# Optimization experiments

Hardware: AMD Instinct MI355X
Metric: run time of the kernel (lower is better)

The kernel has to match this reference:

```python
import jax, jax.numpy as jnp
import numpy as np

NUM_NODES = 20000
NUM_EDGES = 1_000_000
NUM_REL = 12        # internal num_relation (init arg 24 // 2)
NUM_STEP = 6
HID = 128
B_SET = 64          # number of unique (h, r) queries
BS, NEG = 64, 32    # scoring batch
EPS = 1e-10


def setup_inputs() -> dict:
    key = jax.random.key(0)
    ks = jax.random.split(key, 16)
    s = 0.1
    inp = {
        "query_emb": jax.random.normal(ks[0], (2 * NUM_REL + 1, HID), jnp.float32) * s,
        "w_ih": jax.random.normal(ks[1], (4 * HID, HID), jnp.float32) * s,
        "w_hh": jax.random.normal(ks[2], (4 * HID, HID), jnp.float32) * s,
        "b_ih": jax.random.normal(ks[3], (4 * HID,), jnp.float32) * s,
        "b_hh": jax.random.normal(ks[4], (4 * HID,), jnp.float32) * s,
        "wl_w": jax.random.normal(ks[5], (2 * NUM_REL, HID), jnp.float32) * s,
        "wl_b": jax.random.normal(ks[6], (2 * NUM_REL,), jnp.float32) * s,
        "lin_w": jax.random.normal(ks[7], (1, 1), jnp.float32),
        "lin_b": jax.random.normal(ks[8], (1,), jnp.float32),
        "edge_index": jax.random.randint(ks[9], (2, NUM_EDGES), 0, NUM_NODES, jnp.int64),
        "edge_type": jax.random.randint(ks[10], (NUM_EDGES,), 0, 2 * NUM_REL, jnp.int64),
        "h_set": jax.random.randint(ks[11], (B_SET,), 0, NUM_NODES, jnp.int64),
        "r_set": jax.random.randint(ks[12], (B_SET,), 0, NUM_REL, jnp.int64),
        "t_index": jax.random.randint(ks[13], (BS, NEG), 0, NUM_NODES, jnp.int64),
        "hr_inverse": jax.random.randint(ks[14], (BS, NEG), 0, B_SET, jnp.int64),
    }
    return inp


def _lstm(query, w_ih, w_hh, b_ih, b_hh):
    # query: [T, B, D]; single-layer PyTorch LSTM (gate order i, f, g, o)
    B, D = query.shape[1], w_hh.shape[1]
    h0 = jnp.zeros((B, D), query.dtype)

    def step(carry, x):
        h, c = carry
        gates = x @ w_ih.T + b_ih + h @ w_hh.T + b_hh
        i, f, g, o = jnp.split(gates, 4, axis=-1)
        c = jax.nn.sigmoid(f) * c + jax.nn.sigmoid(i) * jnp.tanh(g)
        h = jax.nn.sigmoid(o) * jnp.tanh(c)
        return (h, c), h

    _, hidden = jax.lax.scan(step, (h0, h0), query)
    return hidden  # [T, B, D]


def reference(query_emb, w_ih, w_hh, b_ih, b_hh, wl_w, wl_b, lin_w, lin_b,
              edge_index, edge_type, h_set, r_set, t_index, hr_inverse):
    N1 = NUM_NODES + 1
    B = h_set.shape[0]
    # query sequence: relation repeated (T-1) times, then END token (= NUM_REL)
    q_index = jnp.concatenate(
        [jnp.tile(r_set[None, :], (NUM_STEP - 1, 1)),
         jnp.full((1, B), NUM_REL, dtype=r_set.dtype)], axis=0)  # [T, B]
    query = query_emb[q_index]                                   # [T, B, D]
    hidden = _lstm(query, w_ih, w_hh, b_ih, b_hh)                # [T, B, D]

    memory = jax.nn.one_hot(h_set, N1, dtype=query_emb.dtype)[None]  # [1, B, N1]
    node_in, node_out = edge_index[0], edge_index[1]

    output = None
    for i in range(NUM_STEP):
        k = hidden[i]                 # [B, D]
        v = hidden[: i + 1]           # [i+1, B, D]
        attn = jax.nn.softmax(jnp.einsum('bd,tbd->bt', k, v), axis=-1)
        inp = jnp.einsum('bt,tbn->nb', attn, memory)             # [N1, B]
        weight = jax.nn.softmax(k @ wl_w.T + wl_b, axis=-1).T    # [2R, B]
        # gather -> weight -> scatter_add over edges (edge_weight == 1)
        message = inp[node_in] * weight[edge_type]               # [E, B]
        output = jax.ops.segment_sum(message, node_out, num_segments=N1)
        output = output / jnp.maximum(output.sum(0, keepdims=True), EPS)
        memory = jnp.concatenate([memory, output.T[None]], axis=0)

    score = output[t_index, hr_inverse]           # [BS, NEG]
    return score * lin_w[0, 0] + lin_b[0]
```

## Files before the change

kernel.cpp:

```cpp
#include <hip/hip_runtime.h>
#include <hip/hip_fp16.h>
#include <math.h>

namespace {

constexpr int kN1 = 20001;
constexpr int kNE = 1000000;
constexpr int kNStep = 6;
constexpr int kHid = 128;
constexpr int kB = 64;
constexpr int kNRel2 = 24;
constexpr float kEps = 1e-10f;
constexpr unsigned kSent = (unsigned)kN1;
constexpr int kPMax = kNE + 8 * kN1;
constexpr int kGatherBlocks = 2048;
constexpr int kNWaves = kGatherBlocks * 4;

__device__ __forceinline__ float sig(float x) { return 1.0f / (1.0f + expf(-x)); }

__device__ __forceinline__ float2 cvt2(unsigned u) {
  __half2 h = *reinterpret_cast<__half2*>(&u);
  return __half22float2(h);
}


__global__ __launch_bounds__(256) void lstm_kernel(
    const float* __restrict__ query_emb, const float* __restrict__ w_ih,
    const float* __restrict__ w_hh, const float* __restrict__ b_ih,
    const float* __restrict__ b_hh, const int* __restrict__ r_set,
    float* __restrict__ hidden ) {
  const int b = blockIdx.x;
  const int tid = threadIdx.x;
  __shared__ float xs[kHid], hs[kHid], cs[kHid], gates[4 * kHid];
  if (tid < kHid) { hs[tid] = 0.f; cs[tid] = 0.f; }
  __syncthreads();
  for (int s = 0; s < kNStep; ++s) {
    const int q = (s < kNStep - 1) ? r_set[b] : 12;
    if (tid < kHid) xs[tid] = query_emb[q * kHid + tid];
    __syncthreads();
    for (int j = tid; j < 4 * kHid; j += blockDim.x) {
      const float* wi = &w_ih[j * kHid];
      const float* wh = &w_hh[j * kHid];
      float a = b_ih[j] + b_hh[j];
#pragma unroll 4
      for (int k = 0; k < kHid; ++k) a += xs[k] * wi[k] + hs[k] * wh[k];
      gates[j] = a;
    }
    __syncthreads();
    if (tid < kHid) {
      const float ig = sig(gates[tid]);
      const float fg = sig(gates[kHid + tid]);
      const float gg = tanhf(gates[2 * kHid + tid]);
      const float og = sig(gates[3 * kHid + tid]);
      const float cn = fg * cs[tid] + ig * gg;
      const float hn = og * tanhf(cn);
      cs[tid] = cn;
      hs[tid] = hn;
      hidden[(s * kB + b) * kHid + tid] = hn;
    }
    __syncthreads();
  }
}

__global__ __launch_bounds__(128) void attn_weight_kernel(
    const float* __restrict__ hidden, const float* __restrict__ wl_w,
    const float* __restrict__ wl_b, float* __restrict__ attnAll ,
    float* __restrict__ weightAll ) {
  const int b = blockIdx.x;
  const int tid = threadIdx.x;
  __shared__ float hsm[kNStep][kHid];
  __shared__ float G[kNStep][kNStep];
  __shared__ float logits[kNStep][kNRel2];
  for (int s = 0; s < kNStep; ++s) hsm[s][tid] = hidden[(s * kB + b) * kHid + tid];
  __syncthreads();
  if (tid < 36) {
    const int i = tid / 6, t = tid % 6;
    if (t <= i) {
      float acc = 0.f;
      for (int k = 0; k < kHid; ++k) acc += hsm[i][k] * hsm[t][k];
      G[i][t] = acc;
    }
  }
  for (int p = tid; p < kNStep * kNRel2; p += 128) {
    const int i = p / kNRel2, r = p % kNRel2;
    float acc = wl_b[r];
    for (int k = 0; k < kHid; ++k) acc += hsm[i][k] * wl_w[r * kHid + k];
    logits[i][r] = acc;
  }
  __syncthreads();
  if (tid < kNStep) {
    const int i = tid;
    float m = G[i][0];
    for (int t = 1; t <= i; ++t) m = fmaxf(m, G[i][t]);
    float ssum = 0.f;
    float ev[kNStep];
    for (int t = 0; t <= i; ++t) { ev[t] = expf(G[i][t] - m); ssum += ev[t]; }
    for (int t = 0; t <= i; ++t) attnAll[(i * kNStep + t) * kB + b] = ev[t] / ssum;
    float mw = logits[i][0];
    for (int r = 1; r < kNRel2; ++r) mw = fmaxf(mw, logits[i][r]);
    float sw = 0.f;
    float ew[kNRel2];
    for (int r = 0; r < kNRel2; ++r) { ew[r] = expf(logits[i][r] - mw); sw += ew[r]; }
    for (int r = 0; r < kNRel2; ++r) weightAll[(i * kNRel2 + r) * kB + b] = ew[r] / sw;
  }
}


__global__ __launch_bounds__(256) void zero_kernel(int* __restrict__ counts,
                                                   float* __restrict__ colsumAll) {
  const int i = blockIdx.x * blockDim.x + threadIdx.x;
  if (i < kN1) counts[i] = 0;
  if (i < kNStep * kB) colsumAll[i] = 0.f;
}

__global__ __launch_bounds__(256) void hist_kernel(const int* __restrict__ nout,
                                                   int* __restrict__ counts) {
  for (int e = blockIdx.x * blockDim.x + threadIdx.x; e < kNE;
       e += gridDim.x * blockDim.x)
    atomicAdd(&counts[nout[e]], 1);
}

__global__ __launch_bounds__(1024) void scan_kernel(const int* __restrict__ counts,
                                                    int* __restrict__ poffsets,
                                                    int* __restrict__ cursor) {
  __shared__ int part[1024];
  const int tid = threadIdx.x;
  const int chunk = (kN1 + 1023) / 1024;
  const int beg = tid * chunk;
  const int end = min(beg + chunk, kN1);
  int s = 0;
  for (int i = beg; i < end; ++i) s += (counts[i] + 7) & ~7;
  part[tid] = s;
  __syncthreads();
  for (int off = 1; off < 1024; off <<= 1) {
    const int v = (tid >= off) ? part[tid - off] : 0;
    __syncthreads();
    part[tid] += v;
    __syncthreads();
  }
  int run = part[tid] - s;
  for (int i = beg; i < end; ++i) {
    poffsets[i] = run;
    cursor[i] = run;
    run += (counts[i] + 7) & ~7;
  }
  if (tid == 1023) poffsets[kN1] = part[1023];
}

__global__ __launch_bounds__(256) void fill_kernel(unsigned* __restrict__ packed) {
  for (int i = blockIdx.x * blockDim.x + threadIdx.x; i < kPMax;
       i += gridDim.x * blockDim.x)
    packed[i] = kSent;
}

__global__ __launch_bounds__(256) void permute_kernel(
    const int* __restrict__ nin, const int* __restrict__ nout,
    const int* __restrict__ etype, int* __restrict__ cursor,
    unsigned* __restrict__ packed) {
  for (int e = blockIdx.x * blockDim.x + threadIdx.x; e < kNE;
       e += gridDim.x * blockDim.x) {
    const int d = nout[e];
    const int pos = atomicAdd(&cursor[d], 1);
    packed[pos] = (unsigned)nin[e] | ((unsigned)etype[e] << 15);
  }
}


__global__ __launch_bounds__(256) void inp_kernel(
    const float* __restrict__ attnAll, const float* __restrict__ colsumAll,
    const int* __restrict__ h_set, const float* __restrict__ outs,
    __half* __restrict__ inp, int step) {
  __shared__ float coef[kNStep][kB];
  __shared__ int hsm[kB];
  const int tid = threadIdx.x;
  for (int j = tid; j < kNStep * kB; j += 256) {
    const int t = j >> 6, b = j & 63;
    float c = 0.f;
    if (t == 0)
      c = attnAll[(step * kNStep) * kB + b];
    else if (t <= step)
      c = attnAll[(step * kNStep + t) * kB + b] /
          fmaxf(colsumAll[(t - 1) * kB + b], kEps);
    coef[t][b] = c;
  }
  if (tid < kB) hsm[tid] = h_set[tid];
  __syncthreads();
  const int total = (kN1 + 1) * 16;
  for (int idx = blockIdx.x * blockDim.x + tid; idx < total;
       idx += gridDim.x * blockDim.x) {
    const int n = idx >> 4;
    const int cg = idx & 15;
    float ax = 0.f, ay = 0.f, az = 0.f, aw = 0.f;
    if (n < kN1) {
      for (int t = 1; t <= step; ++t) {
        const float4 ct = *reinterpret_cast<const float4*>(&coef[t][cg * 4]);
        const float4 o = *reinterpret_cast<const float4*>(
            &outs[((long long)(t - 1) * kN1 + n) * kB + cg * 4]);
        ax += ct.x * o.x; ay += ct.y * o.y; az += ct.z * o.z; aw += ct.w * o.w;
      }
      const int c0 = cg * 4;
      if (hsm[c0 + 0] == n) ax += coef[0][c0 + 0];
      if (hsm[c0 + 1] == n) ay += coef[0][c0 + 1];
      if (hsm[c0 + 2] == n) az += coef[0][c0 + 2];
      if (hsm[c0 + 3] == n) aw += coef[0][c0 + 3];
    }
    __half2 h0 = __floats2half2_rn(ax, ay);
    __half2 h1 = __floats2half2_rn(az, aw);
    uint2 u;
    u.x = *reinterpret_cast<unsigned*>(&h0);
    u.y = *reinterpret_cast<unsigned*>(&h1);
    *reinterpret_cast<uint2*>(inp + (long long)idx * 4) = u;
  }
}

__global__ __launch_bounds__(256) void gather_seg_kernel(
    const __half* __restrict__ inp ,
    const float* __restrict__ weight ,
    const unsigned* __restrict__ packed, const int* __restrict__ poffsets,
    float* __restrict__ out, float* __restrict__ colsum) {
  __shared__ __align__(16) __half wsm[kNRel2 * kB];
  __shared__ float red[4][kB];
  const int tid = threadIdx.x;
  const int lane = tid & 63;
  const int wid = tid >> 6;
  const int g = lane >> 3;
  const int cb = lane & 7;
  for (int j = tid; j < kNRel2 * kB; j += 256) wsm[j] = __float2half(weight[j]);
  __syncthreads();

  float csum[8] = {0.f, 0.f, 0.f, 0.f, 0.f, 0.f, 0.f, 0.f};
  const int wave = blockIdx.x * 4 + wid;
  const int P = poffsets[kN1];
  const int nG = P >> 3;
  const int chunkG = (nG + kNWaves - 1) / kNWaves;
  const int gbeg = wave * chunkG;
  if (gbeg < nG) {
    const int gend = min(gbeg + chunkG, nG);
    auto lb = [&](int x) {
      int lo = 0, hi = kN1;
      while (lo < hi) {
        const int mid = (lo + hi) >> 1;
        if (poffsets[mid] < x) lo = mid + 1; else hi = mid;
      }
      return lo;
    };
    const int nbeg = lb(gbeg * 8);
    const int nend = (gend >= nG) ? kN1 : lb(gend * 8);
    if (nbeg < nend) {
      float acc[8] = {0.f, 0.f, 0.f, 0.f, 0.f, 0.f, 0.f, 0.f};
      int n = nbeg;
      int nextB = poffsets[n + 1];
      const int ebeg = poffsets[nbeg];
      const int eend = poffsets[nend];
      for (int ebase = ebeg; ebase < eend; ebase += 8) {
        while (ebase >= nextB) {
#pragma unroll
          for (int j = 0; j < 8; ++j) {
            acc[j] += __shfl_xor(acc[j], 8);
            acc[j] += __shfl_xor(acc[j], 16);
            acc[j] += __shfl_xor(acc[j], 32);
          }
          if (g == 0) {
            *reinterpret_cast<float4*>(out + (long long)n * kB + cb * 8) =
                make_float4(acc[0], acc[1], acc[2], acc[3]);
            *reinterpret_cast<float4*>(out + (long long)n * kB + cb * 8 + 4) =
                make_float4(acc[4], acc[5], acc[6], acc[7]);
#pragma unroll
            for (int j = 0; j < 8; ++j) csum[j] += acc[j];
          }
#pragma unroll
          for (int j = 0; j < 8; ++j) acc[j] = 0.f;
          ++n;
          nextB = poffsets[n + 1];
        }
        const unsigned p = packed[ebase + g];
        const int src = (int)(p & 0x7fffu);
        const int et = (int)(p >> 15);
        const uint4 v4 =
            *reinterpret_cast<const uint4*>(inp + (long long)src * kB + cb * 8);
        const uint4 w4 = *reinterpret_cast<const uint4*>(wsm + et * kB + cb * 8);
        const float2 v0 = cvt2(v4.x), v1 = cvt2(v4.y), v2 = cvt2(v4.z), v3 = cvt2(v4.w);
        const float2 w0 = cvt2(w4.x), w1 = cvt2(w4.y), w2 = cvt2(w4.z), w3 = cvt2(w4.w);
        acc[0] += v0.x * w0.x; acc[1] += v0.y * w0.y;
        acc[2] += v1.x * w1.x; acc[3] += v1.y * w1.y;
        acc[4] += v2.x * w2.x; acc[5] += v2.y * w2.y;
        acc[6] += v3.x * w3.x; acc[7] += v3.y * w3.y;
      }
      while (n < nend) {
#pragma unroll
        for (int j = 0; j < 8; ++j) {
          acc[j] += __shfl_xor(acc[j], 8);
          acc[j] += __shfl_xor(acc[j], 16);
          acc[j] += __shfl_xor(acc[j], 32);
        }
        if (g == 0) {
          *reinterpret_cast<float4*>(out + (long long)n * kB + cb * 8) =
              make_float4(acc[0], acc[1], acc[2], acc[3]);
          *reinterpret_cast<float4*>(out + (long long)n * kB + cb * 8 + 4) =
              make_float4(acc[4], acc[5], acc[6], acc[7]);
#pragma unroll
          for (int j = 0; j < 8; ++j) csum[j] += acc[j];
        }
#pragma unroll
        for (int j = 0; j < 8; ++j) acc[j] = 0.f;
        ++n;
      }
    }
  }
  if (g == 0) {
#pragma unroll
    for (int j = 0; j < 8; ++j) red[wid][cb * 8 + j] = csum[j];
  }
  __syncthreads();
  if (wid == 0) {
    const float r = red[0][lane] + red[1][lane] + red[2][lane] + red[3][lane];
    unsafeAtomicAdd(&colsum[lane], r);
  }
}

__global__ __launch_bounds__(256) void score_kernel(
    const float* __restrict__ outLast, const float* __restrict__ colsumLast,
    const int* __restrict__ t_index, const int* __restrict__ hr_inverse,
    const float* __restrict__ lin_w, const float* __restrict__ lin_b,
    float* __restrict__ out, int n) {
  const int i = blockIdx.x * blockDim.x + threadIdx.x;
  if (i < n) {
    const int node = t_index[i];
    const int b = hr_inverse[i];
    const float v = outLast[(long long)node * kB + b] / fmaxf(colsumLast[b], kEps);
    out[i] = v * lin_w[0] + lin_b[0];
  }
}


__global__ __launch_bounds__(256) void inp_zero_kernel(
    const float* __restrict__ attnAll, const int* __restrict__ h_set,
    const float* __restrict__ outs, float* __restrict__ inp,
    float* __restrict__ out_next, float* __restrict__ colsum, int step) {
  const long long total = (long long)kN1 * kB;
  for (long long idx = (long long)blockIdx.x * blockDim.x + threadIdx.x; idx < total;
       idx += (long long)gridDim.x * blockDim.x) {
    const int b = (int)(idx & 63);
    const int n = (int)(idx >> 6);
    float acc = (h_set[b] == n) ? attnAll[(step * kNStep) * kB + b] : 0.f;
    for (int t = 1; t <= step; ++t)
      acc += attnAll[(step * kNStep + t) * kB + b] *
             outs[(long long)(t - 1) * kN1 * kB + idx];
    inp[idx] = acc;
    out_next[idx] = 0.f;
  }
  if (blockIdx.x == 0 && threadIdx.x < kB) colsum[threadIdx.x] = 0.f;
}

__global__ __launch_bounds__(256) void scatter_kernel(
    const float* __restrict__ inp, const float* __restrict__ weight,
    const int* __restrict__ nin, const int* __restrict__ nout,
    const int* __restrict__ etype, float* __restrict__ out,
    float* __restrict__ colsum) {
  const int lane = threadIdx.x & 63;
  const int wave = blockIdx.x * (blockDim.x >> 6) + (threadIdx.x >> 6);
  const int nwave = gridDim.x * (blockDim.x >> 6);
  __shared__ float wsm[kNRel2 * kB];
  for (int j = threadIdx.x; j < kNRel2 * kB; j += blockDim.x) wsm[j] = weight[j];
  __syncthreads();
  float csum = 0.f;
  for (int e = wave; e < kNE; e += nwave) {
    const float v = inp[(long long)nin[e] * kB + lane] * wsm[etype[e] * kB + lane];
    unsafeAtomicAdd(&out[(long long)nout[e] * kB + lane], v);
    csum += v;
  }
  unsafeAtomicAdd(&colsum[lane], csum);
}

__global__ __launch_bounds__(256) void normalize_kernel(
    float* __restrict__ out, const float* __restrict__ colsum) {
  const long long total = (long long)kN1 * kB;
  for (long long idx = (long long)blockIdx.x * blockDim.x + threadIdx.x; idx < total;
       idx += (long long)gridDim.x * blockDim.x)
    out[idx] /= fmaxf(colsum[idx & 63], kEps);
}

__global__ __launch_bounds__(256) void score_kernel_norm(
    const float* __restrict__ outLast, const int* __restrict__ t_index,
    const int* __restrict__ hr_inverse, const float* __restrict__ lin_w,
    const float* __restrict__ lin_b, float* __restrict__ out, int n) {
  const int i = blockIdx.x * blockDim.x + threadIdx.x;
  if (i < n) {
    out[i] = outLast[(long long)t_index[i] * kB + hr_inverse[i]] * lin_w[0] + lin_b[0];
  }
}

}

extern "C" void kernel_launch(void* const* d_in, const int* in_sizes, int n_in,
                              void* d_out, int out_size, void* d_ws, size_t ws_size,
                              hipStream_t stream) {
  const float* query_emb = (const float*)d_in[0];
  const float* w_ih = (const float*)d_in[1];
  const float* w_hh = (const float*)d_in[2];
  const float* b_ih = (const float*)d_in[3];
  const float* b_hh = (const float*)d_in[4];
  const float* wl_w = (const float*)d_in[5];
  const float* wl_b = (const float*)d_in[6];
  const float* lin_w = (const float*)d_in[7];
  const float* lin_b = (const float*)d_in[8];
  const int* edge_index = (const int*)d_in[9];
  const int* edge_type = (const int*)d_in[10];
  const int* h_set = (const int*)d_in[11];
  const int* r_set = (const int*)d_in[12];
  const int* t_index = (const int*)d_in[13];
  const int* hr_inverse = (const int*)d_in[14];
  float* out = (float*)d_out;

  const int* nin = edge_index;
  const int* nout = edge_index + kNE;

  float* ws = (float*)d_ws;
  float* hidden = ws;
  float* attnAll = hidden + kNStep * kB * kHid;
  float* weightAll = attnAll + kNStep * kNStep * kB;
  float* colsumAll = weightAll + kNStep * kNRel2 * kB;
  float* inpF32 = colsumAll + kNStep * kB;
  __half* inpH = (__half*)inpF32;
  float* outs = inpF32 + (long long)kN1 * kB;
  float* tail = outs + (long long)kNStep * kN1 * kB;
  int* counts = (int*)tail;
  int* poffsets = counts + kN1;
  int* cursor = poffsets + kN1 + 1;
  unsigned* packed = (unsigned*)(cursor + kN1);
  const size_t needed = (size_t)((char*)(packed + kPMax) - (char*)d_ws);

  lstm_kernel<<<kB, 256, 0, stream>>>(query_emb, w_ih, w_hh, b_ih, b_hh, r_set, hidden);
  attn_weight_kernel<<<kB, 128, 0, stream>>>(hidden, wl_w, wl_b, attnAll, weightAll);

  if (ws_size >= needed) {
    zero_kernel<<<(kN1 + 255) / 256, 256, 0, stream>>>(counts, colsumAll);
    hist_kernel<<<1024, 256, 0, stream>>>(nout, counts);
    scan_kernel<<<1, 1024, 0, stream>>>(counts, poffsets, cursor);
    fill_kernel<<<1024, 256, 0, stream>>>(packed);
    permute_kernel<<<1024, 256, 0, stream>>>(nin, nout, edge_type, cursor, packed);

    const int inp_threads = (kN1 + 1) * 16;
    for (int i = 0; i < kNStep; ++i) {
      float* out_i = outs + (long long)i * kN1 * kB;
      inp_kernel<<<(inp_threads + 255) / 256, 256, 0, stream>>>(
          attnAll, colsumAll, h_set, outs, inpH, i);
      gather_seg_kernel<<<kGatherBlocks, 256, 0, stream>>>(
          inpH, weightAll + i * kNRel2 * kB, packed, poffsets, out_i,
          colsumAll + i * kB);
    }
    score_kernel<<<(out_size + 255) / 256, 256, 0, stream>>>(
        outs + 5LL * kN1 * kB, colsumAll + 5 * kB, t_index, hr_inverse, lin_w, lin_b,
        out, out_size);
  } else {
    float* colsum = colsumAll;
    for (int i = 0; i < kNStep; ++i) {
      float* out_i = outs + (long long)i * kN1 * kB;
      inp_zero_kernel<<<2048, 256, 0, stream>>>(attnAll, h_set, outs, inpF32, out_i,
                                                colsum, i);
      scatter_kernel<<<4096, 256, 0, stream>>>(inpF32, weightAll + i * kNRel2 * kB,
                                               nin, nout, edge_type, out_i, colsum);
      normalize_kernel<<<2048, 256, 0, stream>>>(out_i, colsum);
    }
    score_kernel_norm<<<(out_size + 255) / 256, 256, 0, stream>>>(
        outs + 5LL * kN1 * kB, t_index, hr_inverse, lin_w, lin_b, out, out_size);
  }
}
```

Before: 715.9 us.

## Prefetch gathered rows two groups ahead and transpose LSTM weights for coalesced access

The gather/segment-sum loop now handles 16 edges per iteration and software-pipelines the packed-index and fp16 row loads one iteration ahead, so gather latency overlaps with the FMA work. The node-flush logic moves into a shared lambda. Separately, the LSTM weights are transposed into workspace by a new kernel, and a 512-thread LSTM kernel computes one gate per thread with coalesced weight reads. This costs more registers and an extra kernel launch. Out-of-range prefetches use a sentinel row index, which must stay within the inp buffer.

```diff
diff --git a/kernel.cpp b/kernel.cpp
--- a/kernel.cpp
+++ b/kernel.cpp
@@ -24,11 +24,57 @@
 }
 
 
+__global__ __launch_bounds__(256) void transpose_w_kernel(
+    const float* __restrict__ w_ih, const float* __restrict__ w_hh,
+    float* __restrict__ wt) {
+  const int idx = blockIdx.x * 256 + threadIdx.x;
+  if (idx < 256 * 512) {
+    const int k = idx >> 9;
+    const int j = idx & 511;
+    wt[idx] = (k < 128) ? w_ih[j * kHid + k] : w_hh[j * kHid + (k - 128)];
+  }
+}
+
+__global__ __launch_bounds__(512) void lstm_fast_kernel(
+    const float* __restrict__ query_emb, const float* __restrict__ wt,
+    const float* __restrict__ b_ih, const float* __restrict__ b_hh,
+    const int* __restrict__ r_set, float* __restrict__ hidden ) {
+  const int b = blockIdx.x;
+  const int tid = threadIdx.x;
+  __shared__ float xh[256];
+  __shared__ float cst[kHid];
+  __shared__ float gsm[512];
+  const float bias = b_ih[tid] + b_hh[tid];
+  const int q = r_set[b];
+  if (tid < kHid) { cst[tid] = 0.f; xh[kHid + tid] = 0.f; }
+  for (int s = 0; s < kNStep; ++s) {
+    if (tid < kHid) xh[tid] = query_emb[((s < kNStep - 1) ? q : 12) * kHid + tid];
+    __syncthreads();
+    float acc = bias;
+#pragma unroll 8
+    for (int k = 0; k < 256; ++k) acc += xh[k] * wt[k * 512 + tid];
+    gsm[tid] = acc;
+    __syncthreads();
+    if (tid < kHid) {
+      const float ig = sig(gsm[tid]);
+      const float fg = sig(gsm[kHid + tid]);
+      const float gg = tanhf(gsm[2 * kHid + tid]);
+      const float og = sig(gsm[3 * kHid + tid]);
+      const float cn = fg * cst[tid] + ig * gg;
+      cst[tid] = cn;
+      const float hn = og * tanhf(cn);
+      xh[kHid + tid] = hn;
+      hidden[(s * kB + b) * kHid + tid] = hn;
+    }
+    __syncthreads();
+  }
+}
+
 __global__ __launch_bounds__(256) void lstm_kernel(
     const float* __restrict__ query_emb, const float* __restrict__ w_ih,
     const float* __restrict__ w_hh, const float* __restrict__ b_ih,
     const float* __restrict__ b_hh, const int* __restrict__ r_set,
-    float* __restrict__ hidden ) {
+    float* __restrict__ hidden) {
   const int b = blockIdx.x;
   const int tid = threadIdx.x;
   __shared__ float xs[kHid], hs[kHid], cs[kHid], gates[4 * kHid];
@@ -229,6 +275,27 @@
   __syncthreads();
 
   float csum[8] = {0.f, 0.f, 0.f, 0.f, 0.f, 0.f, 0.f, 0.f};
+  float acc[8] = {0.f, 0.f, 0.f, 0.f, 0.f, 0.f, 0.f, 0.f};
+
+  auto flushNode = [&](int node) {
+#pragma unroll
+    for (int j = 0; j < 8; ++j) {
+      acc[j] += __shfl_xor(acc[j], 8);
+      acc[j] += __shfl_xor(acc[j], 16);
+      acc[j] += __shfl_xor(acc[j], 32);
+    }
+    if (g == 0) {
+      *reinterpret_cast<float4*>(out + (long long)node * kB + cb * 8) =
+          make_float4(acc[0], acc[1], acc[2], acc[3]);
+      *reinterpret_cast<float4*>(out + (long long)node * kB + cb * 8 + 4) =
+          make_float4(acc[4], acc[5], acc[6], acc[7]);
+#pragma unroll
+      for (int j = 0; j < 8; ++j) csum[j] += acc[j];
+    }
+#pragma unroll
+    for (int j = 0; j < 8; ++j) acc[j] = 0.f;
+  };
+
   const int wave = blockIdx.x * 4 + wid;
   const int P = poffsets[kN1];
   const int nG = P >> 3;
@@ -247,64 +314,50 @@
     const int nbeg = lb(gbeg * 8);
     const int nend = (gend >= nG) ? kN1 : lb(gend * 8);
     if (nbeg < nend) {
-      float acc[8] = {0.f, 0.f, 0.f, 0.f, 0.f, 0.f, 0.f, 0.f};
       int n = nbeg;
       int nextB = poffsets[n + 1];
       const int ebeg = poffsets[nbeg];
       const int eend = poffsets[nend];
-      for (int ebase = ebeg; ebase < eend; ebase += 8) {
-        while (ebase >= nextB) {
-#pragma unroll
-          for (int j = 0; j < 8; ++j) {
-            acc[j] += __shfl_xor(acc[j], 8);
-            acc[j] += __shfl_xor(acc[j], 16);
-            acc[j] += __shfl_xor(acc[j], 32);
-          }
-          if (g == 0) {
-            *reinterpret_cast<float4*>(out + (long long)n * kB + cb * 8) =
-                make_float4(acc[0], acc[1], acc[2], acc[3]);
-            *reinterpret_cast<float4*>(out + (long long)n * kB + cb * 8 + 4) =
-                make_float4(acc[4], acc[5], acc[6], acc[7]);
-#pragma unroll
-            for (int j = 0; j < 8; ++j) csum[j] += acc[j];
-          }
-#pragma unroll
-          for (int j = 0; j < 8; ++j) acc[j] = 0.f;
-          ++n;
-          nextB = poffsets[n + 1];
+      unsigned pA = (ebeg < eend) ? packed[ebeg + g] : kSent;
+      unsigned pB = (ebeg + 8 < eend) ? packed[ebeg + 8 + g] : kSent;
+      uint4 vA = *reinterpret_cast<const uint4*>(
+          inp + (long long)(pA & 0x7fffu) * kB + cb * 8);
+      uint4 vB = *reinterpret_cast<const uint4*>(
+          inp + (long long)(pB & 0x7fffu) * kB + cb * 8);
+      for (int ebase = ebeg; ebase < eend; ebase += 16) {
+        const bool hasB = (ebase + 8) < eend;
+        const int e2 = ebase + 16, e3 = ebase + 24;
+        const unsigned pC = (e2 < eend) ? packed[e2 + g] : kSent;
+        const unsigned pD = (e3 < eend) ? packed[e3 + g] : kSent;
+        while (ebase >= nextB) { flushNode(n); ++n; nextB = poffsets[n + 1]; }
+        {
+          const uint4 w4 =
+              *reinterpret_cast<const uint4*>(wsm + (pA >> 15) * kB + cb * 8);
+          const float2 v0 = cvt2(vA.x), v1 = cvt2(vA.y), v2 = cvt2(vA.z), v3 = cvt2(vA.w);
+          const float2 w0 = cvt2(w4.x), w1 = cvt2(w4.y), w2 = cvt2(w4.z), w3 = cvt2(w4.w);
+          acc[0] += v0.x * w0.x; acc[1] += v0.y * w0.y;
+          acc[2] += v1.x * w1.x; acc[3] += v1.y * w1.y;
+          acc[4] += v2.x * w2.x; acc[5] += v2.y * w2.y;
+          acc[6] += v3.x * w3.x; acc[7] += v3.y * w3.y;
         }
-        const unsigned p = packed[ebase + g];
-        const int src = (int)(p & 0x7fffu);
-        const int et = (int)(p >> 15);
-        const uint4 v4 =
-            *reinterpret_cast<const uint4*>(inp + (long long)src * kB + cb * 8);
-        const uint4 w4 = *reinterpret_cast<const uint4*>(wsm + et * kB + cb * 8);
-        const float2 v0 = cvt2(v4.x), v1 = cvt2(v4.y), v2 = cvt2(v4.z), v3 = cvt2(v4.w);
-        const float2 w0 = cvt2(w4.x), w1 = cvt2(w4.y), w2 = cvt2(w4.z), w3 = cvt2(w4.w);
-        acc[0] += v0.x * w0.x; acc[1] += v0.y * w0.y;
-        acc[2] += v1.x * w1.x; acc[3] += v1.y * w1.y;
-        acc[4] += v2.x * w2.x; acc[5] += v2.y * w2.y;
-        acc[6] += v3.x * w3.x; acc[7] += v3.y * w3.y;
+        if (hasB) {
+          while (ebase + 8 >= nextB) { flushNode(n); ++n; nextB = poffsets[n + 1]; }
+          const uint4 w4 =
+              *reinterpret_cast<const uint4*>(wsm + (pB >> 15) * kB + cb * 8);
+          const float2 v0 = cvt2(vB.x), v1 = cvt2(vB.y), v2 = cvt2(vB.z), v3 = cvt2(vB.w);
+          const float2 w0 = cvt2(w4.x), w1 = cvt2(w4.y), w2 = cvt2(w4.z), w3 = cvt2(w4.w);
+          acc[0] += v0.x * w0.x; acc[1] += v0.y * w0.y;
+          acc[2] += v1.x * w1.x; acc[3] += v1.y * w1.y;
+          acc[4] += v2.x * w2.x; acc[5] += v2.y * w2.y;
+          acc[6] += v3.x * w3.x; acc[7] += v3.y * w3.y;
+        }
+        pA = pC; pB = pD;
+        vA = *reinterpret_cast<const uint4*>(
+            inp + (long long)(pC & 0x7fffu) * kB + cb * 8);
+        vB = *reinterpret_cast<const uint4*>(
+            inp + (long long)(pD & 0x7fffu) * kB + cb * 8);
       }
-      while (n < nend) {
-#pragma unroll
-        for (int j = 0; j < 8; ++j) {
-          acc[j] += __shfl_xor(acc[j], 8);
-          acc[j] += __shfl_xor(acc[j], 16);
-          acc[j] += __shfl_xor(acc[j], 32);
-        }
-        if (g == 0) {
-          *reinterpret_cast<float4*>(out + (long long)n * kB + cb * 8) =
-              make_float4(acc[0], acc[1], acc[2], acc[3]);
-          *reinterpret_cast<float4*>(out + (long long)n * kB + cb * 8 + 4) =
-              make_float4(acc[4], acc[5], acc[6], acc[7]);
-#pragma unroll
-          for (int j = 0; j < 8; ++j) csum[j] += acc[j];
-        }
-#pragma unroll
-        for (int j = 0; j < 8; ++j) acc[j] = 0.f;
-        ++n;
-      }
+      while (n < nend) { flushNode(n); ++n; }
     }
   }
   if (g == 0) {
@@ -428,12 +481,14 @@
   int* poffsets = counts + kN1;
   int* cursor = poffsets + kN1 + 1;
   unsigned* packed = (unsigned*)(cursor + kN1);
-  const size_t needed = (size_t)((char*)(packed + kPMax) - (char*)d_ws);
-
-  lstm_kernel<<<kB, 256, 0, stream>>>(query_emb, w_ih, w_hh, b_ih, b_hh, r_set, hidden);
-  attn_weight_kernel<<<kB, 128, 0, stream>>>(hidden, wl_w, wl_b, attnAll, weightAll);
+  float* wt = (float*)(packed + kPMax);
+  const size_t needed = (size_t)((char*)(wt + 256 * 512) - (char*)d_ws);
 
   if (ws_size >= needed) {
+    transpose_w_kernel<<<512, 256, 0, stream>>>(w_ih, w_hh, wt);
+    lstm_fast_kernel<<<kB, 512, 0, stream>>>(query_emb, wt, b_ih, b_hh, r_set, hidden);
+    attn_weight_kernel<<<kB, 128, 0, stream>>>(hidden, wl_w, wl_b, attnAll, weightAll);
+
     zero_kernel<<<(kN1 + 255) / 256, 256, 0, stream>>>(counts, colsumAll);
     hist_kernel<<<1024, 256, 0, stream>>>(nout, counts);
     scan_kernel<<<1, 1024, 0, stream>>>(counts, poffsets, cursor);
@@ -453,6 +508,9 @@
         outs + 5LL * kN1 * kB, colsumAll + 5 * kB, t_index, hr_inverse, lin_w, lin_b,
         out, out_size);
   } else {
+    lstm_kernel<<<kB, 256, 0, stream>>>(query_emb, w_ih, w_hh, b_ih, b_hh, r_set,
+                                        hidden);
+    attn_weight_kernel<<<kB, 128, 0, stream>>>(hidden, wl_w, wl_b, attnAll, weightAll);
     float* colsum = colsumAll;
     for (int i = 0; i < kNStep; ++i) {
       float* out_i = outs + (long long)i * kN1 * kB;
```

After: 669.7 us. -6.5%, faster.
